# Kernel tuning notes

Measured on AMD Instinct MI355X. Metric: run time of the kernel, lower is better.

## Reference

```python
import jax, jax.numpy as jnp
import numpy as np
import math

D = 32   # in_planes / d_model
T = 9    # num_contexts
L = 24   # token_len
H = 8    # nhead
HD = D // H
NEUMANN = 3
ALPHA = 0.9

def _lin(x, w, b):
    return x @ w.T + b

def _gelu(x):
    return jax.nn.gelu(x, approximate=False)

def reference(x, ln_g, ln_b, rp_w1, rp_b1, rp_w2, rp_b2, W_causal,
              mask_w, mask_b, val_w1, val_b1, val_w2, val_b2, fuse_gate,
              q_w, q_b, k_w, k_b, v_w, v_b, m_w, m_b,
              W_logit, W_ctx, rel_pos_bias, pre_prompt, conv_w, conv_b, p_w, p_b):
    b = x.shape[0]
    x_btlc = jnp.transpose(x, (0, 2, 3, 1))              # (b,t,l,c)
    # ---- rule pooling (LayerNorm -> Linear -> GELU -> Linear) ----
    pooled = x_btlc.mean(axis=(1, 2))                    # (b,c)
    mu = pooled.mean(-1, keepdims=True)
    var = pooled.var(-1, keepdims=True)
    pn = (pooled - mu) / jnp.sqrt(var + 1e-5) * ln_g + ln_b
    pooled_rule = _lin(_gelu(_lin(pn, rp_w1, rp_b1)), rp_w2, rp_b2)
    # ---- causal graph discovery ----
    A = jax.nn.softplus(W_causal) * (1.0 - jnp.eye(D, dtype=x.dtype))
    # ---- intervention engine ----
    x_obs = x_btlc.mean(axis=(1, 2))                     # (b,c)
    scale = jnp.clip(jnp.std(x_btlc, axis=(1, 2), ddof=1), 1e-3)  # torch unbiased std
    M = jax.nn.sigmoid(_lin(pooled_rule, mask_w, mask_b))
    v_raw = _lin(_gelu(_lin(pooled_rule, val_w1, val_b1)), val_w2, val_b2)
    v32 = jnp.tanh(v_raw) * scale + x_obs
    x_do = (1.0 - M) * x_obs + M * v32
    A32 = ALPHA * A / (A.sum(-1, keepdims=True) + 1e-6)  # row-normalize
    y = x_do
    for _ in range(NEUMANN):                             # fp32 Neumann series
        y = x_do + y @ A32.T
    delta = (y - x_obs)[:, None, None, :]
    fused = x_btlc + jax.nn.sigmoid(fuse_gate) * delta   # (b,t,l,c)
    # ---- cosine-sim multi-head attention with rel-pos bias & head mixing ----
    def heads(w, bb):
        h = _lin(fused, w, bb).reshape(b, T, L, H, HD).transpose(0, 1, 3, 2, 4)
        return h / jnp.linalg.norm(h, axis=-1, keepdims=True).clip(1e-12)
    q = heads(q_w, q_b); k = heads(k_w, k_b); v = heads(v_w, v_b)
    logits = jnp.einsum('bthid,bthjd->bthij', q, k) / math.sqrt(HD)
    idx = jnp.arange(L)
    rel = jnp.clip(idx[:, None] - idx[None, :] + (L - 1), 0, 2 * L - 2)
    logits = logits + rel_pos_bias[:, rel][None, None]   # (h,L,L) broadcast
    logits = jnp.einsum('bthij,hH->btHij', logits, W_logit)
    atten = jax.nn.softmax(logits, axis=-1)
    atten = jnp.einsum('bthij,hH->btHij', atten, W_ctx)
    x_att = jnp.einsum('bthij,bthjd->bthid', atten, v)
    x_att = _lin(x_att.transpose(0, 1, 3, 2, 4).reshape(b, T, L, D), m_w, m_b)
    x_att = jnp.transpose(x_att, (0, 3, 1, 2))           # (b,c,t,l)
    # ---- prediction branch (conv over contexts + linear over tokens) ----
    pre = jnp.broadcast_to(pre_prompt, (b, D, 1, L))
    con = jnp.concatenate([x_att[:, :, :T - 1], pre], axis=2)   # (b,c,T,L)
    p = jax.lax.conv_general_dilated(con, conv_w, (1, 1), 'VALID',
        dimension_numbers=('NCHW', 'OIHW', 'NCHW')) + conv_b[None, :, None, None]
    p = jax.nn.relu(p)                                   # ConvNormAct act; norm=identity at init
    p = _lin(p, p_w, p_b)                                # Linear(token_len, token_len)
    p = x_att[:, :, T - 1:] - p
    return jnp.concatenate([x_att[:, :, :T - 1], p], axis=2)


def setup_inputs() -> dict:
    key = jax.random.key(0)
    ks = jax.random.split(key, 24)
    B = 4096
    def r(i, sh, s=0.02):
        return jax.random.normal(ks[i], sh, jnp.float32) * s
    return dict(
        x=jax.random.normal(ks[0], (B, D, T, L), jnp.float32),
        ln_g=jnp.ones((D,), jnp.float32), ln_b=jnp.zeros((D,), jnp.float32),
        rp_w1=r(1, (D, D)), rp_b1=jnp.zeros((D,), jnp.float32),
        rp_w2=r(2, (D, D)), rp_b2=jnp.zeros((D,), jnp.float32),
        W_causal=r(3, (D, D)),
        mask_w=r(4, (D, D)), mask_b=jnp.zeros((D,), jnp.float32),
        val_w1=r(5, (D, D)), val_b1=jnp.zeros((D,), jnp.float32),
        val_w2=r(6, (D, D)), val_b2=jnp.zeros((D,), jnp.float32),
        fuse_gate=jnp.float32(0.5),
        q_w=r(7, (D, D)), q_b=jnp.zeros((D,), jnp.float32),
        k_w=r(8, (D, D)), k_b=jnp.zeros((D,), jnp.float32),
        v_w=r(9, (D, D)), v_b=jnp.zeros((D,), jnp.float32),
        m_w=r(10, (D, D)), m_b=jnp.zeros((D,), jnp.float32),
        W_logit=jnp.eye(H, dtype=jnp.float32) + r(11, (H, H), 0.01),
        W_ctx=jnp.eye(H, dtype=jnp.float32) + r(12, (H, H), 0.01),
        rel_pos_bias=r(13, (H, 2 * L - 1)),
        pre_prompt=r(14, (1, D, 1, L)),
        conv_w=r(15, (D, D, T, 1)), conv_b=jnp.zeros((D,), jnp.float32),
        p_w=r(16, (L, L)), p_b=jnp.zeros((L,), jnp.float32),
    )
```

## Files before the change

### kernel.cpp

```cpp
#include <hip/hip_runtime.h>
#include <hip/hip_bf16.h>

#define DD 32
#define TT 9
#define LL 24
#define HH 8
#define NPOS 216
#define RPB_W 47
#define ALPHA 0.9f

__device__ __forceinline__ float gelu_exact(float x) {
    return 0.5f * x * (1.0f + erff(x * 0.7071067811865476f));
}
__device__ __forceinline__ float sigmoidf_(float x) { return 1.0f / (1.0f + expf(-x)); }


__global__ void k0_prep(const float* __restrict__ wcausal,
                        const float* __restrict__ w_logit,
                        const float* __restrict__ rpb,
                        float* __restrict__ ws) {
    __shared__ float A[DD][DD];
    __shared__ float rs[DD];
    int tid = threadIdx.x;
    int i = tid >> 5, j = tid & 31;
    float a = (i == j) ? 0.0f : log1pf(expf(wcausal[tid]));
    A[i][j] = a;
    __syncthreads();
    if (j == 0) {
        float s = 0.0f;
        for (int k = 0; k < DD; k++) s += A[i][k];
        rs[i] = ALPHA / (s + 1e-6f);
    }
    __syncthreads();
    ws[tid] = A[i][j] * rs[i];
    if (tid < 64) ws[1024 + tid] = 0.5f * w_logit[tid];
    if (tid < 384) {
        int H = tid / 48, r = tid % 48;
        float v = 0.0f;
        if (r < RPB_W) {
            for (int h = 0; h < HH; h++) v += w_logit[h * HH + H] * rpb[h * RPB_W + r];
        }
        ws[1088 + tid] = v;
    }
}

__global__ __launch_bounds__(256) void k1a(const float* __restrict__ x,
                                           float* __restrict__ sp, float* __restrict__ sq) {
    int b = blockIdx.x, tid = threadIdx.x;
    int c = tid >> 3, r = tid & 7;
    const float4* x4 = (const float4*)(x + (size_t)b * (DD * NPOS) + (size_t)c * NPOS);
    float s = 0.0f, q = 0.0f;
    for (int k = r; k < 54; k += 8) {
        float4 v = x4[k];
        s += v.x + v.y + v.z + v.w;
        q += v.x * v.x + v.y * v.y + v.z * v.z + v.w * v.w;
    }
    for (int m = 1; m < 8; m <<= 1) { s += __shfl_xor(s, m); q += __shfl_xor(q, m); }
    if (r == 0) { sp[b * DD + c] = s; sq[b * DD + c] = q; }
}

__global__ __launch_bounds__(64) void k1b(
    const float* __restrict__ ln_g, const float* __restrict__ ln_b,
    const float* __restrict__ rp_w1, const float* __restrict__ rp_b1,
    const float* __restrict__ rp_w2, const float* __restrict__ rp_b2,
    const float* __restrict__ mask_w, const float* __restrict__ mask_b,
    const float* __restrict__ val_w1, const float* __restrict__ val_b1,
    const float* __restrict__ val_w2, const float* __restrict__ val_b2,
    const float* __restrict__ fuse_gate, const float* __restrict__ ws,
    float* __restrict__ sp , const float* __restrict__ sq)
{
    __shared__ float W[6][1024];
    __shared__ float V[7][32];
    int tid = threadIdx.x;
    for (int idx = tid; idx < 1024; idx += 64) {
        W[0][idx] = rp_w1[idx]; W[1][idx] = rp_w2[idx]; W[2][idx] = mask_w[idx];
        W[3][idx] = val_w1[idx]; W[4][idx] = val_w2[idx]; W[5][idx] = ws[idx];
    }
    if (tid < 32) {
        V[0][tid] = ln_g[tid]; V[1][tid] = ln_b[tid]; V[2][tid] = rp_b1[tid];
        V[3][tid] = rp_b2[tid]; V[4][tid] = mask_b[tid]; V[5][tid] = val_b1[tid];
        V[6][tid] = val_b2[tid];
    }
    __syncthreads();
    int b = blockIdx.x * 64 + tid;

    float pooled[32], scl[32];
    const float4* sp4 = (const float4*)(sp + (size_t)b * 32);
    const float4* sq4 = (const float4*)(sq + (size_t)b * 32);
    #pragma unroll
    for (int k = 0; k < 8; k++) {
        float4 sv = sp4[k], qv = sq4[k];
        float ss[4] = {sv.x, sv.y, sv.z, sv.w};
        float qq[4] = {qv.x, qv.y, qv.z, qv.w};
        #pragma unroll
        for (int m = 0; m < 4; m++) {
            int c = 4 * k + m;
            float p = ss[m] * (1.0f / NPOS);
            pooled[c] = p;
            float var1 = (qq[m] - (float)NPOS * p * p) * (1.0f / (NPOS - 1));
            scl[c] = fmaxf(sqrtf(fmaxf(var1, 0.0f)), 1e-3f);
        }
    }
    float mu = 0.0f;
    #pragma unroll
    for (int c = 0; c < 32; c++) mu += pooled[c];
    mu *= (1.0f / 32.0f);
    float vv = 0.0f;
    #pragma unroll
    for (int c = 0; c < 32; c++) { float d = pooled[c] - mu; vv += d * d; }
    vv *= (1.0f / 32.0f);
    float inv = rsqrtf(vv + 1e-5f);
    float pn[32];
    #pragma unroll
    for (int c = 0; c < 32; c++) pn[c] = (pooled[c] - mu) * inv * V[0][c] + V[1][c];

    float h1[32];
    #pragma unroll
    for (int i = 0; i < 32; i++) {
        float acc = V[2][i];
        #pragma unroll
        for (int j = 0; j < 32; j++) acc += pn[j] * W[0][i * 32 + j];
        h1[i] = gelu_exact(acc);
    }
    float pr[32];
    #pragma unroll
    for (int i = 0; i < 32; i++) {
        float acc = V[3][i];
        #pragma unroll
        for (int j = 0; j < 32; j++) acc += h1[j] * W[1][i * 32 + j];
        pr[i] = acc;
    }
    float g1[32];
    #pragma unroll
    for (int i = 0; i < 32; i++) {
        float acc = V[5][i];
        #pragma unroll
        for (int j = 0; j < 32; j++) acc += pr[j] * W[3][i * 32 + j];
        g1[i] = gelu_exact(acc);
    }
    float xd[32];
    #pragma unroll
    for (int i = 0; i < 32; i++) {
        float am = V[4][i];
        #pragma unroll
        for (int j = 0; j < 32; j++) am += pr[j] * W[2][i * 32 + j];
        float M = sigmoidf_(am);
        float av = V[6][i];
        #pragma unroll
        for (int j = 0; j < 32; j++) av += g1[j] * W[4][i * 32 + j];
        float v32 = tanhf(av) * scl[i] + pooled[i];
        xd[i] = (1.0f - M) * pooled[i] + M * v32;
    }
    float y[32];
    #pragma unroll
    for (int c = 0; c < 32; c++) y[c] = xd[c];
    for (int it = 0; it < 3; it++) {
        float ny[32];
        #pragma unroll
        for (int i = 0; i < 32; i++) {
            float acc = xd[i];
            #pragma unroll
            for (int j = 0; j < 32; j++) acc += y[j] * W[5][i * 32 + j];
            ny[i] = acc;
        }
        #pragma unroll
        for (int c = 0; c < 32; c++) y[c] = ny[c];
    }
    float g = sigmoidf_(fuse_gate[0]);
    float4* dout4 = (float4*)(sp + (size_t)b * 32);
    #pragma unroll
    for (int k = 0; k < 8; k++) {
        float4 o;
        o.x = g * (y[4 * k + 0] - pooled[4 * k + 0]);
        o.y = g * (y[4 * k + 1] - pooled[4 * k + 1]);
        o.z = g * (y[4 * k + 2] - pooled[4 * k + 2]);
        o.w = g * (y[4 * k + 3] - pooled[4 * k + 3]);
        dout4[k] = o;
    }
}

__global__ __launch_bounds__(256) void k2_attn(
    const float* __restrict__ x,
    const float* __restrict__ ws,
    const float* __restrict__ delta,
    const float* __restrict__ q_w, const float* __restrict__ q_b,
    const float* __restrict__ k_w, const float* __restrict__ k_b,
    const float* __restrict__ v_w, const float* __restrict__ v_b,
    const float* __restrict__ m_w, const float* __restrict__ m_b,
    const float* __restrict__ w_ctx,
    float* __restrict__ out)
{
    __shared__ float r1[3456];
    __shared__ float r2[5832];
    __shared__ float msc[640];
    float* fusedf = r1;
    float* qsf = r1 + 864;
    float* ksf = r1 + 1728;
    float* vsf = r1 + 2592;
    float* wqf = r2;
    float* wkf = r2 + 1024;
    float* wvf = r2 + 2048;
    float* lgf = r2;
    float* wmf = r2 + 4808;
    float* bqf = msc, *bkf = msc + 32, *bvf = msc + 64, *bmf = msc + 96;
    float* wl05f = msc + 128;
    float* wcf = msc + 192;
    float* rpmf = msc + 256;

    int blk = blockIdx.x;
    int b = blk / TT, t = blk % TT;
    int tid = threadIdx.x;

    for (int idx = tid; idx < 768; idx += 256) {
        int m = idx >> 8, r = idx & 255;
        int i = r >> 3, jq = r & 7;
        const float* src = (m == 0) ? q_w : (m == 1) ? k_w : v_w;
        float* dst = (m == 0) ? wqf : (m == 1) ? wkf : wvf;
        float4 v = ((const float4*)src)[r];
        dst[(4 * jq + 0) * 32 + i] = v.x;
        dst[(4 * jq + 1) * 32 + i] = v.y;
        dst[(4 * jq + 2) * 32 + i] = v.z;
        dst[(4 * jq + 3) * 32 + i] = v.w;
    }
    if (tid < 32) { bqf[tid] = q_b[tid]; bkf[tid] = k_b[tid]; bvf[tid] = v_b[tid]; bmf[tid] = m_b[tid]; }
    else if (tid < 96) wl05f[tid - 32] = ws[1024 + tid - 32];
    else if (tid < 160) wcf[tid - 96] = w_ctx[tid - 96];
    for (int idx = tid; idx < 384; idx += 256) rpmf[idx] = ws[1088 + idx];
    if (tid < 192) {
        int c = tid / 6, k = tid % 6;
        const float4* p = (const float4*)(x + (size_t)b * (DD * NPOS) + (size_t)c * NPOS + t * LL);
        float4 v = p[k];
        float gd = delta[b * DD + c];
        int l0 = 4 * k;
        fusedf[(l0 + 0) * 36 + c] = v.x + gd;
        fusedf[(l0 + 1) * 36 + c] = v.y + gd;
        fusedf[(l0 + 2) * 36 + c] = v.z + gd;
        fusedf[(l0 + 3) * 36 + c] = v.w + gd;
    }
    __syncthreads();

    if (tid < 192) {
        int l = tid >> 3, q = tid & 7;
        float4 aq = *(const float4*)&bqf[4 * q];
        float4 ak = *(const float4*)&bkf[4 * q];
        float4 av = *(const float4*)&bvf[4 * q];
        #pragma unroll
        for (int j = 0; j < 32; j++) {
            float f = fusedf[l * 36 + j];
            float4 w0 = *(const float4*)&wqf[j * 32 + 4 * q];
            float4 w1 = *(const float4*)&wkf[j * 32 + 4 * q];
            float4 w2 = *(const float4*)&wvf[j * 32 + 4 * q];
            aq.x += f * w0.x; aq.y += f * w0.y; aq.z += f * w0.z; aq.w += f * w0.w;
            ak.x += f * w1.x; ak.y += f * w1.y; ak.z += f * w1.z; ak.w += f * w1.w;
            av.x += f * w2.x; av.y += f * w2.y; av.z += f * w2.z; av.w += f * w2.w;
        }
        float nq = 1.0f / fmaxf(sqrtf(aq.x*aq.x + aq.y*aq.y + aq.z*aq.z + aq.w*aq.w), 1e-12f);
        float nk = 1.0f / fmaxf(sqrtf(ak.x*ak.x + ak.y*ak.y + ak.z*ak.z + ak.w*ak.w), 1e-12f);
        float nv = 1.0f / fmaxf(sqrtf(av.x*av.x + av.y*av.y + av.z*av.z + av.w*av.w), 1e-12f);
        aq.x *= nq; aq.y *= nq; aq.z *= nq; aq.w *= nq;
        ak.x *= nk; ak.y *= nk; ak.z *= nk; ak.w *= nk;
        av.x *= nv; av.y *= nv; av.z *= nv; av.w *= nv;
        *(float4*)&qsf[l * 36 + 4 * q] = aq;
        *(float4*)&ksf[l * 36 + 4 * q] = ak;
        *(float4*)&vsf[l * 36 + 4 * q] = av;
    }
    __syncthreads();

    {
        int idx = tid;
        int i = idx >> 3, jq = idx & 7;
        float4 v = ((const float4*)m_w)[idx];
        wmf[(4 * jq + 0) * 32 + i] = v.x;
        wmf[(4 * jq + 1) * 32 + i] = v.y;
        wmf[(4 * jq + 2) * 32 + i] = v.z;
        wmf[(4 * jq + 3) * 32 + i] = v.w;
    }
    if (tid < 192) {
        int h = tid / 24, i2 = tid % 24;
        float4 q4 = *(const float4*)&qsf[i2 * 36 + 4 * h];
        float row[24];
        #pragma unroll
        for (int j = 0; j < 24; j++) {
            float4 k4 = *(const float4*)&ksf[j * 36 + 4 * h];
            row[j] = q4.x * k4.x + q4.y * k4.y + q4.z * k4.z + q4.w * k4.w;
        }
        #pragma unroll
        for (int j = 0; j < 24; j++) lgf[h * 601 + i2 * 25 + j] = row[j];
    }
    __syncthreads();

    for (int ij = tid; ij < 576; ij += 256) {
        int i = ij / 24, j = ij - i * 24;
        int off = i * 25 + j;
        int rel = i - j + (LL - 1);
        float tmp[8];
        #pragma unroll
        for (int h = 0; h < 8; h++) tmp[h] = lgf[h * 601 + off];
        #pragma unroll
        for (int H = 0; H < 8; H++) {
            float a = rpmf[H * 48 + rel];
            #pragma unroll
            for (int h = 0; h < 8; h++) a += tmp[h] * wl05f[h * 8 + H];
            lgf[H * 601 + off] = a;
        }
    }
    __syncthreads();

    if (tid < 192) {
        int H = tid / 24, i = tid % 24;
        float* rp = &lgf[H * 601 + i * 25];
        float mx = -1e30f;
        #pragma unroll
        for (int j = 0; j < 24; j++) mx = fmaxf(mx, rp[j]);
        float s = 0.0f;
        #pragma unroll
        for (int j = 0; j < 24; j++) { float e = __expf(rp[j] - mx); rp[j] = e; s += e; }
        float inv = 1.0f / s;
        #pragma unroll
        for (int j = 0; j < 24; j++) rp[j] *= inv;
    }
    __syncthreads();

    for (int ij = tid; ij < 576; ij += 256) {
        int i = ij / 24, j = ij - i * 24;
        int off = i * 25 + j;
        float tmp[8];
        #pragma unroll
        for (int h = 0; h < 8; h++) tmp[h] = lgf[h * 601 + off];
        #pragma unroll
        for (int H = 0; H < 8; H++) {
            float a = 0.0f;
            #pragma unroll
            for (int h = 0; h < 8; h++) a += tmp[h] * wcf[h * 8 + H];
            lgf[H * 601 + off] = a;
        }
    }
    __syncthreads();

    if (tid < 192) {
        int l = tid >> 3, q = tid & 7;
        float4 acc = {0.0f, 0.0f, 0.0f, 0.0f};
        #pragma unroll
        for (int j = 0; j < 24; j++) {
            float a = lgf[q * 601 + l * 25 + j];
            float4 v4 = *(const float4*)&vsf[j * 36 + 4 * q];
            acc.x += a * v4.x; acc.y += a * v4.y; acc.z += a * v4.z; acc.w += a * v4.w;
        }
        *(float4*)&fusedf[l * 36 + 4 * q] = acc;
    }
    __syncthreads();

    if (tid < 192) {
        int l = tid >> 3, q = tid & 7;
        float4 acc = *(const float4*)&bmf[4 * q];
        #pragma unroll
        for (int c = 0; c < 32; c++) {
            float f = fusedf[l * 36 + c];
            float4 w4 = *(const float4*)&wmf[c * 32 + 4 * q];
            acc.x += f * w4.x; acc.y += f * w4.y; acc.z += f * w4.z; acc.w += f * w4.w;
        }
        float* resf = qsf;
        resf[(4 * q + 0) * 25 + l] = acc.x;
        resf[(4 * q + 1) * 25 + l] = acc.y;
        resf[(4 * q + 2) * 25 + l] = acc.z;
        resf[(4 * q + 3) * 25 + l] = acc.w;
    }
    __syncthreads();

    if (tid < 192) {
        const float* resf = qsf;
        int c = tid / 6, k = tid - c * 6;
        float4 v;
        v.x = resf[c * 25 + 4 * k + 0];
        v.y = resf[c * 25 + 4 * k + 1];
        v.z = resf[c * 25 + 4 * k + 2];
        v.w = resf[c * 25 + 4 * k + 3];
        float4* o4 = (float4*)(out + (size_t)b * (DD * NPOS) + (size_t)c * NPOS + t * LL);
        o4[k] = v;
    }
}

__global__ __launch_bounds__(256) void k3_pred(
    const float* __restrict__ pre_prompt,
    const float* __restrict__ conv_w, const float* __restrict__ conv_b,
    const float* __restrict__ p_w, const float* __restrict__ p_b,
    float* __restrict__ out)
{
    __shared__ float conf[DD * NPOS];
    __shared__ __hip_bfloat16 cwh[DD * 292];
    __shared__ float pbuff[DD * 25];
    __shared__ __hip_bfloat16 pwh[576];
    __shared__ float pbv[24], cbv[32];
    int b = blockIdx.x, tid = threadIdx.x;

    const float4* o4 = (const float4*)(out + (size_t)b * (DD * NPOS));
    for (int idx = tid; idx < 1728; idx += 256) {
        int flat = idx * 4;
        int t = (flat % NPOS) / LL;
        float4 v;
        if (t < 8) {
            v = o4[idx];
        } else {
            int c = flat / NPOS, l = flat % LL;
            v = ((const float4*)pre_prompt)[(c * LL + l) >> 2];
        }
        conf[flat + 0] = v.x; conf[flat + 1] = v.y; conf[flat + 2] = v.z; conf[flat + 3] = v.w;
    }
    for (int idx = tid; idx < 2304; idx += 256) {
        float4 v = ((const float4*)conv_w)[idx];
        int flat = idx * 4;
        float vv[4] = {v.x, v.y, v.z, v.w};
        #pragma unroll
        for (int e = 0; e < 4; e++) {
            int f = flat + e;
            int co = f / 288, r = f - co * 288;
            cwh[co * 292 + r] = __float2bfloat16(vv[e]);
        }
    }
    for (int idx = tid; idx < 144; idx += 256) {
        float4 v = ((const float4*)p_w)[idx];
        pwh[idx * 4 + 0] = __float2bfloat16(v.x);
        pwh[idx * 4 + 1] = __float2bfloat16(v.y);
        pwh[idx * 4 + 2] = __float2bfloat16(v.z);
        pwh[idx * 4 + 3] = __float2bfloat16(v.w);
    }
    if (tid < 24) pbv[tid] = p_b[tid];
    if (tid >= 32 && tid < 64) cbv[tid - 32] = conv_b[tid - 32];
    __syncthreads();

    if (tid < 192) {
        int co = tid / 6, ql = tid - co * 6;
        float cb = cbv[co];
        float4 acc = {cb, cb, cb, cb};
        for (int ci = 0; ci < 32; ci++) {
            #pragma unroll
            for (int tt = 0; tt < 9; tt++) {
                float w = __bfloat162float(cwh[co * 292 + ci * 9 + tt]);
                float4 v = *(const float4*)&conf[ci * NPOS + tt * LL + ql * 4];
                acc.x += w * v.x; acc.y += w * v.y; acc.z += w * v.z; acc.w += w * v.w;
            }
        }
        pbuff[co * 25 + 4 * ql + 0] = fmaxf(acc.x, 0.0f);
        pbuff[co * 25 + 4 * ql + 1] = fmaxf(acc.y, 0.0f);
        pbuff[co * 25 + 4 * ql + 2] = fmaxf(acc.z, 0.0f);
        pbuff[co * 25 + 4 * ql + 3] = fmaxf(acc.w, 0.0f);
    }
    __syncthreads();

    if (tid < 192) {
        int c = tid / 6, ql = tid - c * 6;
        float4 acc = {pbv[4 * ql + 0], pbv[4 * ql + 1], pbv[4 * ql + 2], pbv[4 * ql + 3]};
        #pragma unroll
        for (int lp = 0; lp < 24; lp++) {
            float pv = pbuff[c * 25 + lp];
            acc.x += pv * __bfloat162float(pwh[(4 * ql + 0) * 24 + lp]);
            acc.y += pv * __bfloat162float(pwh[(4 * ql + 1) * 24 + lp]);
            acc.z += pv * __bfloat162float(pwh[(4 * ql + 2) * 24 + lp]);
            acc.w += pv * __bfloat162float(pwh[(4 * ql + 3) * 24 + lp]);
        }
        float4* op = (float4*)(out + (size_t)b * (DD * NPOS) + (size_t)c * NPOS + 8 * LL);
        float4 xa = op[ql];
        float4 r;
        r.x = xa.x - acc.x; r.y = xa.y - acc.y; r.z = xa.z - acc.z; r.w = xa.w - acc.w;
        op[ql] = r;
    }
}

extern "C" void kernel_launch(void* const* d_in, const int* in_sizes, int n_in,
                              void* d_out, int out_size, void* d_ws, size_t ws_size,
                              hipStream_t stream) {
    const float* x        = (const float*)d_in[0];
    const float* ln_g     = (const float*)d_in[1];
    const float* ln_b     = (const float*)d_in[2];
    const float* rp_w1    = (const float*)d_in[3];
    const float* rp_b1    = (const float*)d_in[4];
    const float* rp_w2    = (const float*)d_in[5];
    const float* rp_b2    = (const float*)d_in[6];
    const float* W_causal = (const float*)d_in[7];
    const float* mask_w   = (const float*)d_in[8];
    const float* mask_b   = (const float*)d_in[9];
    const float* val_w1   = (const float*)d_in[10];
    const float* val_b1   = (const float*)d_in[11];
    const float* val_w2   = (const float*)d_in[12];
    const float* val_b2   = (const float*)d_in[13];
    const float* fuse_g   = (const float*)d_in[14];
    const float* q_w      = (const float*)d_in[15];
    const float* q_b      = (const float*)d_in[16];
    const float* k_w      = (const float*)d_in[17];
    const float* k_b      = (const float*)d_in[18];
    const float* v_w      = (const float*)d_in[19];
    const float* v_b      = (const float*)d_in[20];
    const float* m_w      = (const float*)d_in[21];
    const float* m_b      = (const float*)d_in[22];
    const float* W_logit  = (const float*)d_in[23];
    const float* W_ctx    = (const float*)d_in[24];
    const float* rel_pb   = (const float*)d_in[25];
    const float* pre_pr   = (const float*)d_in[26];
    const float* conv_w   = (const float*)d_in[27];
    const float* conv_b   = (const float*)d_in[28];
    const float* p_w      = (const float*)d_in[29];
    const float* p_b      = (const float*)d_in[30];
    float* out = (float*)d_out;

    int B = in_sizes[0] / (DD * NPOS);

    float* ws = (float*)d_ws;
    float* sp = ws + 2048;
    float* sq = sp + (size_t)B * 32;

    hipLaunchKernelGGL(k0_prep, dim3(1), dim3(1024), 0, stream, W_causal, W_logit, rel_pb, ws);
    hipLaunchKernelGGL(k1a, dim3(B), dim3(256), 0, stream, x, sp, sq);
    hipLaunchKernelGGL(k1b, dim3(B / 64), dim3(64), 0, stream,
                       ln_g, ln_b, rp_w1, rp_b1, rp_w2, rp_b2,
                       mask_w, mask_b, val_w1, val_b1, val_w2, val_b2,
                       fuse_g, ws, sp, sq);
    hipLaunchKernelGGL(k2_attn, dim3(B * TT), dim3(256), 0, stream,
                       x, ws, sp, q_w, q_b, k_w, k_b, v_w, v_b, m_w, m_b,
                       W_ctx, out);
    hipLaunchKernelGGL(k3_pred, dim3(B), dim3(256), 0, stream,
                       pre_pr, conv_w, conv_b, p_w, p_b, out);
}
```

Measured before the change: 1.081 ms.

## Rewrite attention kernel with bf16 MFMA and per-batch context loop

Rewrites the attention stage so the QKV projection, QK logits, PV product and output projection use bf16 16x16x32 MFMA instructions, with softmax done through cross-lane shuffles. Each block now handles one batch element and loops over the nine contexts, so weights are loaded into shared memory once per batch rather than once per context. The head-mixing matrices are folded into the K scaling and into the probability mixing. Activations and weights are rounded to bf16, which costs accuracy, and the grid is nine times smaller, which reduces parallelism.

```diff
diff --git a/kernel.cpp b/kernel.cpp
--- a/kernel.cpp
+++ b/kernel.cpp
@@ -9,10 +9,24 @@
 #define RPB_W 47
 #define ALPHA 0.9f
 
+typedef __attribute__((ext_vector_type(8))) short short8x;
+typedef __attribute__((ext_vector_type(4))) float float4x;
+
 __device__ __forceinline__ float gelu_exact(float x) {
     return 0.5f * x * (1.0f + erff(x * 0.7071067811865476f));
 }
 __device__ __forceinline__ float sigmoidf_(float x) { return 1.0f / (1.0f + expf(-x)); }
+
+__device__ __forceinline__ short f2b(float f) {
+    union { float f; unsigned u; } x; x.f = f;
+    unsigned r = x.u + 0x7fffu + ((x.u >> 16) & 1u);
+    return (short)(r >> 16);
+}
+__device__ __forceinline__ float b2f(short s) {
+    union { unsigned u; float f; } x;
+    x.u = ((unsigned)(unsigned short)s) << 16;
+    return x.f;
+}
 
 
 __global__ void k0_prep(const float* __restrict__ wcausal,
@@ -179,7 +193,7 @@
     }
 }
 
-__global__ __launch_bounds__(256) void k2_attn(
+__global__ __launch_bounds__(256, 4) void k2_attn(
     const float* __restrict__ x,
     const float* __restrict__ ws,
     const float* __restrict__ delta,
@@ -190,193 +204,190 @@
     const float* __restrict__ w_ctx,
     float* __restrict__ out)
 {
-    __shared__ float r1[3456];
-    __shared__ float r2[5832];
-    __shared__ float msc[640];
-    float* fusedf = r1;
-    float* qsf = r1 + 864;
-    float* ksf = r1 + 1728;
-    float* vsf = r1 + 2592;
-    float* wqf = r2;
-    float* wkf = r2 + 1024;
-    float* wvf = r2 + 2048;
-    float* lgf = r2;
-    float* wmf = r2 + 4808;
-    float* bqf = msc, *bkf = msc + 32, *bvf = msc + 64, *bmf = msc + 96;
-    float* wl05f = msc + 128;
-    float* wcf = msc + 192;
-    float* rpmf = msc + 256;
-
-    int blk = blockIdx.x;
-    int b = blk / TT, t = blk % TT;
+    __shared__ __align__(16) short shF[1024];
+    __shared__ __align__(16) short shW[3072];
+    __shared__ __align__(16) short shQ[1024];
+    __shared__ __align__(16) short shK[1024];
+    __shared__ __align__(16) short shVT[1024];
+    __shared__ __align__(16) short shP[8192];
+    __shared__ __align__(16) short shXA[1024];
+    __shared__ __align__(16) short shMW[1024];
+    __shared__ float shMisc[672];
+
+    int b = blockIdx.x;
     int tid = threadIdx.x;
+    int wv = tid >> 6, lane = tid & 63, quad = lane >> 4, c16 = lane & 15;
 
     for (int idx = tid; idx < 768; idx += 256) {
-        int m = idx >> 8, r = idx & 255;
-        int i = r >> 3, jq = r & 7;
-        const float* src = (m == 0) ? q_w : (m == 1) ? k_w : v_w;
-        float* dst = (m == 0) ? wqf : (m == 1) ? wkf : wvf;
-        float4 v = ((const float4*)src)[r];
-        dst[(4 * jq + 0) * 32 + i] = v.x;
-        dst[(4 * jq + 1) * 32 + i] = v.y;
-        dst[(4 * jq + 2) * 32 + i] = v.z;
-        dst[(4 * jq + 3) * 32 + i] = v.w;
-    }
-    if (tid < 32) { bqf[tid] = q_b[tid]; bkf[tid] = k_b[tid]; bvf[tid] = v_b[tid]; bmf[tid] = m_b[tid]; }
-    else if (tid < 96) wl05f[tid - 32] = ws[1024 + tid - 32];
-    else if (tid < 160) wcf[tid - 96] = w_ctx[tid - 96];
-    for (int idx = tid; idx < 384; idx += 256) rpmf[idx] = ws[1088 + idx];
-    if (tid < 192) {
-        int c = tid / 6, k = tid % 6;
-        const float4* p = (const float4*)(x + (size_t)b * (DD * NPOS) + (size_t)c * NPOS + t * LL);
-        float4 v = p[k];
-        float gd = delta[b * DD + c];
-        int l0 = 4 * k;
-        fusedf[(l0 + 0) * 36 + c] = v.x + gd;
-        fusedf[(l0 + 1) * 36 + c] = v.y + gd;
-        fusedf[(l0 + 2) * 36 + c] = v.z + gd;
-        fusedf[(l0 + 3) * 36 + c] = v.w + gd;
+        const float* src = (idx < 256) ? q_w : (idx < 512) ? k_w : v_w;
+        float4 v = ((const float4*)src)[idx & 255];
+        short4 s4; s4.x = f2b(v.x); s4.y = f2b(v.y); s4.z = f2b(v.z); s4.w = f2b(v.w);
+        *(short4*)&shW[idx * 4] = s4;
+    }
+    {
+        float4 v = ((const float4*)m_w)[tid];
+        short4 s4; s4.x = f2b(v.x); s4.y = f2b(v.y); s4.z = f2b(v.z); s4.w = f2b(v.w);
+        *(short4*)&shMW[tid * 4] = s4;
+    }
+    for (int idx = tid; idx < 672; idx += 256) {
+        float v;
+        if (idx < 384)      v = ws[1088 + idx];
+        else if (idx < 448) v = ws[1024 + idx - 384];
+        else if (idx < 512) v = w_ctx[idx - 448];
+        else if (idx < 544) v = q_b[idx - 512];
+        else if (idx < 576) v = k_b[idx - 544];
+        else if (idx < 608) v = v_b[idx - 576];
+        else if (idx < 640) v = m_b[idx - 608];
+        else                v = delta[(size_t)b * 32 + idx - 640];
+        shMisc[idx] = v;
+    }
+    {
+        shF[768 + tid] = 0;
+        int n = tid >> 3, jj = 24 + (tid & 7);
+        shVT[n * 32 + jj] = 0;
     }
     __syncthreads();
 
-    if (tid < 192) {
-        int l = tid >> 3, q = tid & 7;
-        float4 aq = *(const float4*)&bqf[4 * q];
-        float4 ak = *(const float4*)&bkf[4 * q];
-        float4 av = *(const float4*)&bvf[4 * q];
-        #pragma unroll
-        for (int j = 0; j < 32; j++) {
-            float f = fusedf[l * 36 + j];
-            float4 w0 = *(const float4*)&wqf[j * 32 + 4 * q];
-            float4 w1 = *(const float4*)&wkf[j * 32 + 4 * q];
-            float4 w2 = *(const float4*)&wvf[j * 32 + 4 * q];
-            aq.x += f * w0.x; aq.y += f * w0.y; aq.z += f * w0.z; aq.w += f * w0.w;
-            ak.x += f * w1.x; ak.y += f * w1.y; ak.z += f * w1.z; ak.w += f * w1.w;
-            av.x += f * w2.x; av.y += f * w2.y; av.z += f * w2.z; av.w += f * w2.w;
-        }
-        float nq = 1.0f / fmaxf(sqrtf(aq.x*aq.x + aq.y*aq.y + aq.z*aq.z + aq.w*aq.w), 1e-12f);
-        float nk = 1.0f / fmaxf(sqrtf(ak.x*ak.x + ak.y*ak.y + ak.z*ak.z + ak.w*ak.w), 1e-12f);
-        float nv = 1.0f / fmaxf(sqrtf(av.x*av.x + av.y*av.y + av.z*av.z + av.w*av.w), 1e-12f);
-        aq.x *= nq; aq.y *= nq; aq.z *= nq; aq.w *= nq;
-        ak.x *= nk; ak.y *= nk; ak.z *= nk; ak.w *= nk;
-        av.x *= nv; av.y *= nv; av.z *= nv; av.w *= nv;
-        *(float4*)&qsf[l * 36 + 4 * q] = aq;
-        *(float4*)&ksf[l * 36 + 4 * q] = ak;
-        *(float4*)&vsf[l * 36 + 4 * q] = av;
-    }
-    __syncthreads();
-
-    {
-        int idx = tid;
-        int i = idx >> 3, jq = idx & 7;
-        float4 v = ((const float4*)m_w)[idx];
-        wmf[(4 * jq + 0) * 32 + i] = v.x;
-        wmf[(4 * jq + 1) * 32 + i] = v.y;
-        wmf[(4 * jq + 2) * 32 + i] = v.z;
-        wmf[(4 * jq + 3) * 32 + i] = v.w;
-    }
-    if (tid < 192) {
-        int h = tid / 24, i2 = tid % 24;
-        float4 q4 = *(const float4*)&qsf[i2 * 36 + 4 * h];
-        float row[24];
-        #pragma unroll
-        for (int j = 0; j < 24; j++) {
-            float4 k4 = *(const float4*)&ksf[j * 36 + 4 * h];
-            row[j] = q4.x * k4.x + q4.y * k4.y + q4.z * k4.z + q4.w * k4.w;
-        }
-        #pragma unroll
-        for (int j = 0; j < 24; j++) lgf[h * 601 + i2 * 25 + j] = row[j];
-    }
-    __syncthreads();
-
-    for (int ij = tid; ij < 576; ij += 256) {
-        int i = ij / 24, j = ij - i * 24;
-        int off = i * 25 + j;
-        int rel = i - j + (LL - 1);
-        float tmp[8];
-        #pragma unroll
-        for (int h = 0; h < 8; h++) tmp[h] = lgf[h * 601 + off];
-        #pragma unroll
-        for (int H = 0; H < 8; H++) {
-            float a = rpmf[H * 48 + rel];
+    for (int t = 0; t < TT; t++) {
+        if (tid < 192) {
+            int c = tid / 6, k6 = tid % 6;
+            float4 v = *(const float4*)(x + (size_t)b * (DD * NPOS) + (size_t)c * NPOS + t * LL + 4 * k6);
+            float dl = shMisc[640 + c];
+            int l0 = 4 * k6;
+            shF[(l0 + 0) * 32 + c] = f2b(v.x + dl);
+            shF[(l0 + 1) * 32 + c] = f2b(v.y + dl);
+            shF[(l0 + 2) * 32 + c] = f2b(v.z + dl);
+            shF[(l0 + 3) * 32 + c] = f2b(v.w + dl);
+        }
+        __syncthreads();
+
+        {
+            int tm = wv >> 1;
+            short8x afrag = *(short8x*)&shF[(16 * tm + c16) * 32 + quad * 8];
             #pragma unroll
-            for (int h = 0; h < 8; h++) a += tmp[h] * wl05f[h * 8 + H];
-            lgf[H * 601 + off] = a;
-        }
-    }
-    __syncthreads();
-
-    if (tid < 192) {
-        int H = tid / 24, i = tid % 24;
-        float* rp = &lgf[H * 601 + i * 25];
-        float mx = -1e30f;
-        #pragma unroll
-        for (int j = 0; j < 24; j++) mx = fmaxf(mx, rp[j]);
-        float s = 0.0f;
-        #pragma unroll
-        for (int j = 0; j < 24; j++) { float e = __expf(rp[j] - mx); rp[j] = e; s += e; }
-        float inv = 1.0f / s;
-        #pragma unroll
-        for (int j = 0; j < 24; j++) rp[j] *= inv;
-    }
-    __syncthreads();
-
-    for (int ij = tid; ij < 576; ij += 256) {
-        int i = ij / 24, j = ij - i * 24;
-        int off = i * 25 + j;
-        float tmp[8];
-        #pragma unroll
-        for (int h = 0; h < 8; h++) tmp[h] = lgf[h * 601 + off];
-        #pragma unroll
-        for (int H = 0; H < 8; H++) {
-            float a = 0.0f;
+            for (int s = 0; s < 3; s++) {
+                int tn = (wv & 1) * 3 + s;
+                short8x bfrag = *(short8x*)&shW[(16 * tn + c16) * 32 + quad * 8];
+                float4x acc = {0.0f, 0.0f, 0.0f, 0.0f};
+                acc = __builtin_amdgcn_mfma_f32_16x16x32_bf16(afrag, bfrag, acc, 0, 0, 0);
+                int gc = 16 * tn + c16;
+                float bias = shMisc[512 + gc];
+                #pragma unroll
+                for (int e = 0; e < 4; e++) {
+                    float d = acc[e] + bias;
+                    float ss = d * d;
+                    ss += __shfl_xor(ss, 1);
+                    ss += __shfl_xor(ss, 2);
+                    float val = d / fmaxf(sqrtf(ss), 1e-12f);
+                    int gr = 16 * tm + quad * 4 + e;
+                    if (gc < 32)      shQ[gr * 32 + gc] = f2b(val);
+                    else if (gc < 64) shK[gr * 32 + (gc - 32)] = f2b(val);
+                    else if (gr < 24) shVT[(gc - 64) * 32 + gr] = f2b(val);
+                }
+            }
+        }
+        __syncthreads();
+
+        {
+            short8x aq0 = *(short8x*)&shQ[c16 * 32 + quad * 8];
+            short8x aq1 = *(short8x*)&shQ[(16 + c16) * 32 + quad * 8];
+            short8x bk0 = *(short8x*)&shK[c16 * 32 + quad * 8];
+            short8x bk1 = *(short8x*)&shK[(16 + c16) * 32 + quad * 8];
             #pragma unroll
-            for (int h = 0; h < 8; h++) a += tmp[h] * wcf[h * 8 + H];
-            lgf[H * 601 + off] = a;
-        }
-    }
-    __syncthreads();
-
-    if (tid < 192) {
-        int l = tid >> 3, q = tid & 7;
-        float4 acc = {0.0f, 0.0f, 0.0f, 0.0f};
-        #pragma unroll
-        for (int j = 0; j < 24; j++) {
-            float a = lgf[q * 601 + l * 25 + j];
-            float4 v4 = *(const float4*)&vsf[j * 36 + 4 * q];
-            acc.x += a * v4.x; acc.y += a * v4.y; acc.z += a * v4.z; acc.w += a * v4.w;
-        }
-        *(float4*)&fusedf[l * 36 + 4 * q] = acc;
-    }
-    __syncthreads();
-
-    if (tid < 192) {
-        int l = tid >> 3, q = tid & 7;
-        float4 acc = *(const float4*)&bmf[4 * q];
-        #pragma unroll
-        for (int c = 0; c < 32; c++) {
-            float f = fusedf[l * 36 + c];
-            float4 w4 = *(const float4*)&wmf[c * 32 + 4 * q];
-            acc.x += f * w4.x; acc.y += f * w4.y; acc.z += f * w4.z; acc.w += f * w4.w;
-        }
-        float* resf = qsf;
-        resf[(4 * q + 0) * 25 + l] = acc.x;
-        resf[(4 * q + 1) * 25 + l] = acc.y;
-        resf[(4 * q + 2) * 25 + l] = acc.z;
-        resf[(4 * q + 3) * 25 + l] = acc.w;
-    }
-    __syncthreads();
-
-    if (tid < 192) {
-        const float* resf = qsf;
-        int c = tid / 6, k = tid - c * 6;
-        float4 v;
-        v.x = resf[c * 25 + 4 * k + 0];
-        v.y = resf[c * 25 + 4 * k + 1];
-        v.z = resf[c * 25 + 4 * k + 2];
-        v.w = resf[c * 25 + 4 * k + 3];
-        float4* o4 = (float4*)(out + (size_t)b * (DD * NPOS) + (size_t)c * NPOS + t * LL);
-        o4[k] = v;
+            for (int hh = 0; hh < 2; hh++) {
+                int H = 2 * wv + hh;
+                float s0 = shMisc[384 + (2 * quad) * 8 + H];
+                float s1 = shMisc[384 + (2 * quad + 1) * 8 + H];
+                short8x bs0, bs1;
+                #pragma unroll
+                for (int j = 0; j < 8; j++) {
+                    float sc = (j < 4) ? s0 : s1;
+                    bs0[j] = f2b(b2f(bk0[j]) * sc);
+                    bs1[j] = f2b(b2f(bk1[j]) * sc);
+                }
+                float4x l00 = {0,0,0,0}, l01 = {0,0,0,0}, l10 = {0,0,0,0}, l11 = {0,0,0,0};
+                l00 = __builtin_amdgcn_mfma_f32_16x16x32_bf16(aq0, bs0, l00, 0, 0, 0);
+                l01 = __builtin_amdgcn_mfma_f32_16x16x32_bf16(aq0, bs1, l01, 0, 0, 0);
+                l10 = __builtin_amdgcn_mfma_f32_16x16x32_bf16(aq1, bs0, l10, 0, 0, 0);
+                l11 = __builtin_amdgcn_mfma_f32_16x16x32_bf16(aq1, bs1, l11, 0, 0, 0);
+                #pragma unroll
+                for (int tmm = 0; tmm < 2; tmm++) {
+                    float4x la = tmm ? l10 : l00;
+                    float4x lb = tmm ? l11 : l01;
+                    int j1 = 16 + c16;
+                    #pragma unroll
+                    for (int e = 0; e < 4; e++) {
+                        int i = 16 * tmm + quad * 4 + e;
+                        float v0 = la[e] + shMisc[H * 48 + min(i - c16 + 23, 47)];
+                        float v1 = (j1 < 24) ? (lb[e] + shMisc[H * 48 + min(i - j1 + 23, 47)])
+                                             : -1e30f;
+                        float m = fmaxf(v0, v1);
+                        m = fmaxf(m, __shfl_xor(m, 1));
+                        m = fmaxf(m, __shfl_xor(m, 2));
+                        m = fmaxf(m, __shfl_xor(m, 4));
+                        m = fmaxf(m, __shfl_xor(m, 8));
+                        float e0 = __expf(v0 - m);
+                        float e1 = __expf(v1 - m);
+                        float s = e0 + e1;
+                        s += __shfl_xor(s, 1);
+                        s += __shfl_xor(s, 2);
+                        s += __shfl_xor(s, 4);
+                        s += __shfl_xor(s, 8);
+                        float inv = 1.0f / s;
+                        shP[H * 1024 + i * 32 + c16]      = f2b(e0 * inv);
+                        shP[H * 1024 + i * 32 + 16 + c16] = f2b(e1 * inv);
+                    }
+                }
+            }
+        }
+        __syncthreads();
+
+        {
+            int tmm = wv & 1, tnn = wv >> 1;
+            short8x vfrag = *(short8x*)&shVT[(16 * tnn + c16) * 32 + quad * 8];
+            short8x zfr = {0, 0, 0, 0, 0, 0, 0, 0};
+            int hn = 4 * tnn + (c16 >> 2);
+            float4x pacc = {0.0f, 0.0f, 0.0f, 0.0f};
+            #pragma unroll
+            for (int hx = 0; hx < 4; hx++) {
+                int H = 4 * tnn + hx;
+                float accf[8] = {0, 0, 0, 0, 0, 0, 0, 0};
+                #pragma unroll
+                for (int h = 0; h < 8; h++) {
+                    short8x ph = *(short8x*)&shP[h * 1024 + (16 * tmm + c16) * 32 + quad * 8];
+                    float w = shMisc[448 + h * 8 + H];
+                    #pragma unroll
+                    for (int j = 0; j < 8; j++) accf[j] += w * b2f(ph[j]);
+                }
+                short8x pa;
+                #pragma unroll
+                for (int j = 0; j < 8; j++) pa[j] = f2b(accf[j]);
+                short8x bmk = (hn == H) ? vfrag : zfr;
+                pacc = __builtin_amdgcn_mfma_f32_16x16x32_bf16(pa, bmk, pacc, 0, 0, 0);
+            }
+            #pragma unroll
+            for (int e = 0; e < 4; e++)
+                shXA[(16 * tmm + quad * 4 + e) * 32 + 16 * tnn + c16] = f2b(pacc[e]);
+        }
+        __syncthreads();
+
+        {
+            int tm6 = wv & 1, tn6 = wv >> 1;
+            short8x axa = *(short8x*)&shXA[(16 * tm6 + c16) * 32 + quad * 8];
+            short8x bmw = *(short8x*)&shMW[(16 * tn6 + c16) * 32 + quad * 8];
+            float4x oacc = {0.0f, 0.0f, 0.0f, 0.0f};
+            oacc = __builtin_amdgcn_mfma_f32_16x16x32_bf16(axa, bmw, oacc, 0, 0, 0);
+            int oc = 16 * tn6 + c16;
+            int r0 = 16 * tm6 + quad * 4;
+            if (r0 < 24) {
+                float bmv = shMisc[608 + oc];
+                float4 o;
+                o.x = oacc[0] + bmv; o.y = oacc[1] + bmv;
+                o.z = oacc[2] + bmv; o.w = oacc[3] + bmv;
+                *(float4*)(out + (size_t)b * (DD * NPOS) + (size_t)oc * NPOS + t * LL + r0) = o;
+            }
+        }
+        __syncthreads();
     }
 }
 
@@ -514,7 +525,7 @@
                        ln_g, ln_b, rp_w1, rp_b1, rp_w2, rp_b2,
                        mask_w, mask_b, val_w1, val_b1, val_w2, val_b2,
                        fuse_g, ws, sp, sq);
-    hipLaunchKernelGGL(k2_attn, dim3(B * TT), dim3(256), 0, stream,
+    hipLaunchKernelGGL(k2_attn, dim3(B), dim3(256), 0, stream,
                        x, ws, sp, q_w, q_b, k_w, k_b, v_w, v_b, m_w, m_b,
                        W_ctx, out);
     hipLaunchKernelGGL(k3_pred, dim3(B), dim3(256), 0, stream,
```

Measured after the change: 1.519 ms. +40.5%, slower.
